# Kernel tuning notes

Hardware: AMD Instinct MI355X
Metric: run time of the kernel (lower is better)

Reference implementation:

```python
import jax, jax.numpy as jnp
import numpy as np

ALPHA = 0.5
PATH_LEN = 7  # 1 start entity + 3 (module, entity) hops
NUM_ENTITIES = 200000
EMBED = 128
NUM_MOD = 64
HIDDEN = 512
OUT_DIM = 64
BATCH = 8192


def setup_inputs() -> dict:
    key = jax.random.key(0)
    ks = jax.random.split(key, 8)
    stdv = 1.0 / np.sqrt(EMBED)
    return {
        "entity_embeds": jax.random.normal(ks[0], (NUM_ENTITIES, EMBED), jnp.float32) * 0.05,
        "W_mods": jax.random.uniform(ks[1], (NUM_MOD, EMBED, EMBED), jnp.float32, -stdv, stdv),
        "W1": jax.random.normal(ks[2], (HIDDEN, EMBED), jnp.float32) * stdv,
        "b1": jax.random.normal(ks[3], (HIDDEN,), jnp.float32) * 0.01,
        "W2": jax.random.normal(ks[4], (OUT_DIM, HIDDEN), jnp.float32) * (1.0 / np.sqrt(HIDDEN)),
        "b2": jax.random.normal(ks[5], (OUT_DIM,), jnp.float32) * 0.01,
        "entity_ids": jax.random.randint(ks[6], (BATCH, 4), 0, NUM_ENTITIES, jnp.int64 if jax.config.jax_enable_x64 else jnp.int32),
        "module_ids": jax.random.randint(ks[7], (BATCH, 3), 0, NUM_MOD, jnp.int64 if jax.config.jax_enable_x64 else jnp.int32),
    }


def reference(entity_embeds, W_mods, W1, b1, W2, b2, entity_ids, module_ids):
    # Batched version of ModuleNet.forward over a batch of fixed-length-7 paths.
    x = entity_embeds[entity_ids[:, 0]]  # [B, E] start entity embedding
    bias = x
    for h in range(3):  # hops over (module_id, entity_id) pairs
        Wm = W_mods[module_ids[:, h]]          # [B, E, E] per-row weight gather
        bias = entity_embeds[entity_ids[:, h + 1]]  # [B, E]
        x = jax.nn.relu(jnp.einsum('boi,bi->bo', Wm, x) + bias)
    w = 1.0 / (PATH_LEN * ALPHA)
    out = (1.0 - w) * bias + w * x  # [B, E]
    # classifier: Linear -> ReLU -> Linear
    h1 = jax.nn.relu(out @ W1.T + b1)
    logits = h1 @ W2.T + b2  # [B, OUT_DIM]
    return logits
```

## Files before the change

### kernel.cpp

```cpp
#include <hip/hip_runtime.h>

namespace {

typedef short bf16x8 __attribute__((ext_vector_type(8)));
typedef float f32x4 __attribute__((ext_vector_type(4)));

constexpr int BATCH = 8192;
constexpr int NMOD  = 64;
constexpr int CAP   = 256;
constexpr int CSTR  = 16;
constexpr float WB  = 1.0f / (7.0f * 0.5f);

constexpr size_t OFF_XH0 = 0;
constexpr size_t OFF_XL0 = 524288;
constexpr size_t OFF_XH1 = 1048576;
constexpr size_t OFF_XL1 = 1572864;
constexpr size_t OFF_W1H = 2097152;
constexpr size_t OFF_W1L = 2129920;
constexpr size_t OFF_W2H = 2162688;
constexpr size_t OFF_W2L = 2179072;
constexpr size_t OFF_CNT = 2195456;
constexpr size_t OFF_BKT = 2198528;

__device__ __forceinline__ ushort f2bf(float x) {
  unsigned u = __builtin_bit_cast(unsigned, x);
  u += 0x7FFFu + ((u >> 16) & 1u);
  return (ushort)(u >> 16);
}
__device__ __forceinline__ float bf2f(ushort h) {
  return __builtin_bit_cast(float, ((unsigned)h) << 16);
}
__device__ __forceinline__ void cvt8(const float* v, bf16x8& hi, bf16x8& lo) {
#pragma unroll
  for (int j = 0; j < 8; ++j) {
    const float x = v[j];
    const ushort h = f2bf(x);
    hi[j] = (short)h;
    lo[j] = (short)f2bf(x - bf2f(h));
  }
}

__global__ __launch_bounds__(256) void k_prep(const float* __restrict__ W1,
                                              const float* __restrict__ W2,
                                              const int* __restrict__ mids,
                                              float* __restrict__ ws) {
  __shared__ int wsum[4];
  const int bx = blockIdx.x;
  const int tid = threadIdx.x;
  if (bx < 48) {
    const float* src;
    ushort *dh, *dl;
    size_t i8;
    if (bx < 32) {
      src = W1; dh = (ushort*)(ws + OFF_W1H); dl = (ushort*)(ws + OFF_W1L);
      i8 = (size_t)bx * 256 + tid;
    } else {
      src = W2; dh = (ushort*)(ws + OFF_W2H); dl = (ushort*)(ws + OFF_W2L);
      i8 = (size_t)(bx - 32) * 256 + tid;
    }
    float v[8];
    *(float4*)&v[0] = *(const float4*)&src[i8 * 8];
    *(float4*)&v[4] = *(const float4*)&src[i8 * 8 + 4];
    bf16x8 hi, lo;
    cvt8(v, hi, lo);
    *(bf16x8*)&dh[i8 * 8] = hi;
    *(bf16x8*)&dl[i8 * 8] = lo;
  } else {
    const int hm = bx - 48;
    const int h = hm >> 6, m = hm & 63;
    int* cnt = (int*)(ws + OFF_CNT);
    int* bkt = (int*)(ws + OFF_BKT) + hm * CAP;
    const int wv = tid >> 6, ln = tid & 63;
    int count = 0;
    for (int it = 0; it < BATCH / 256; ++it) {
      const int b = it * 256 + tid;
      const bool hit = (mids[b * 3 + h] == m);
      const unsigned long long mask = __ballot(hit);
      const int pre = __popcll(mask & ((1ull << ln) - 1ull));
      if (ln == 0) wsum[wv] = __popcll(mask);
      __syncthreads();
      int wbase = count;
#pragma unroll
      for (int u = 0; u < 4; ++u)
        if (u < wv) wbase += wsum[u];
      if (hit) bkt[wbase + pre] = b;
      count += wsum[0] + wsum[1] + wsum[2] + wsum[3];
      __syncthreads();
    }
    if (tid == 0) cnt[hm * CSTR] = count;
  }
}

template <int HOP>
__global__ __launch_bounds__(256, 2) void k_hop(const float* __restrict__ E,
                                                const float* __restrict__ Wm,
                                                const int* __restrict__ eids,
                                                float* __restrict__ ws) {
  const int m = blockIdx.x >> 3, sl = blockIdx.x & 7;
  const int cn = ((const int*)(ws + OFF_CNT))[(HOP * NMOD + m) * CSTR];
  const int r0 = sl * 32;
  if (r0 >= cn) return;
  const int nr = min(32, cn - r0);

  __shared__ ushort wh[128 * 72];
  __shared__ ushort wl[128 * 72];
  __shared__ int rows[32], esrc[32], ebia[32];

  const int tid = threadIdx.x;
  const float* WmG = Wm + (size_t)m * 16384;
  const int* bkt = (const int*)(ws + OFF_BKT) + (HOP * NMOD + m) * CAP + r0;
  const ushort* XHp = (const ushort*)(ws + (HOP == 2 ? OFF_XH1 : OFF_XH0));
  const ushort* XLp = (const ushort*)(ws + (HOP == 2 ? OFF_XL1 : OFF_XL0));
  ushort* XHn = (ushort*)(ws + (HOP == 1 ? OFF_XH1 : OFF_XH0));
  ushort* XLn = (ushort*)(ws + (HOP == 1 ? OFF_XL1 : OFF_XL0));

  if (tid < 32) {
    const int b = bkt[tid < nr ? tid : 0];
    rows[tid] = b;
    esrc[tid] = (HOP == 0) ? eids[b * 4] : b;
    ebia[tid] = eids[b * 4 + HOP + 1];
  }

  const int w = tid >> 6, l = tid & 63;
  const int lg = l >> 4, lr = l & 15;
  const int g = w & 1, f0 = (w >> 1) * 4;
  const int row = g * 16 + lr;

  f32x4 acc[4] = {};

#pragma unroll
  for (int p = 0; p < 2; ++p) {
    __syncthreads();
    for (int e = tid; e < 128 * 8; e += 256) {
      const int c = e >> 3, s = e & 7;
      float v[8];
      const float* sp = &WmG[(size_t)c * 128 + p * 64 + s * 8];
      *(float4*)&v[0] = *(const float4*)&sp[0];
      *(float4*)&v[4] = *(const float4*)&sp[4];
      bf16x8 hi, lo;
      cvt8(v, hi, lo);
      *(bf16x8*)&wh[c * 72 + s * 8] = hi;
      *(bf16x8*)&wl[c * 72 + s * 8] = lo;
    }
    __syncthreads();

    bf16x8 ah[2], al[2];
#pragma unroll
    for (int s = 0; s < 2; ++s) {
      const int k0 = p * 64 + s * 32 + lg * 8;
      if (HOP == 0) {
        const float* sp = E + (size_t)esrc[row] * 128;
        float v[8];
        *(float4*)&v[0] = *(const float4*)&sp[k0];
        *(float4*)&v[4] = *(const float4*)&sp[k0 + 4];
        cvt8(v, ah[s], al[s]);
      } else {
        const size_t xo = (size_t)esrc[row] * 128 + k0;
        ah[s] = *(const bf16x8*)&XHp[xo];
        al[s] = *(const bf16x8*)&XLp[xo];
      }
    }

#pragma unroll
    for (int f = 0; f < 4; ++f) {
      const int c = (f0 + f) * 16 + lr;
#pragma unroll
      for (int s = 0; s < 2; ++s) {
        const bf16x8 bh = *(const bf16x8*)&wh[c * 72 + s * 32 + lg * 8];
        const bf16x8 bl = *(const bf16x8*)&wl[c * 72 + s * 32 + lg * 8];
        acc[f] = __builtin_amdgcn_mfma_f32_16x16x32_bf16(ah[s], bh, acc[f], 0, 0, 0);
        acc[f] = __builtin_amdgcn_mfma_f32_16x16x32_bf16(al[s], bh, acc[f], 0, 0, 0);
        acc[f] = __builtin_amdgcn_mfma_f32_16x16x32_bf16(ah[s], bl, acc[f], 0, 0, 0);
      }
    }
  }

#pragma unroll
  for (int q = 0; q < 4; ++q) {
    const int orow = g * 16 + lg * 4 + q;
    if (orow < nr) {
      const int b = rows[orow];
      const float* bp = E + (size_t)ebia[orow] * 128;
      const size_t ob = (size_t)b * 128;
#pragma unroll
      for (int f = 0; f < 4; ++f) {
        const int col = (f0 + f) * 16 + lr;
        const float bias = bp[col];
        float v = fmaxf(acc[f][q] + bias, 0.f);
        if (HOP == 2) v = (1.f - WB) * bias + WB * v;
        const ushort h = f2bf(v);
        XHn[ob + col] = h;
        XLn[ob + col] = f2bf(v - bf2f(h));
      }
    }
  }
}

constexpr int HSTR = 520;
__global__ __launch_bounds__(256, 2) void k_mlp(const float* __restrict__ b1,
                                                const float* __restrict__ b2,
                                                float* __restrict__ ws,
                                                float* __restrict__ out) {
  __shared__ ushort hh[16 * HSTR];
  __shared__ ushort hl[16 * HSTR];
  const int tid = threadIdx.x;
  const int row0 = blockIdx.x * 16;
  const ushort* XH = (const ushort*)(ws + OFF_XH0);
  const ushort* XL = (const ushort*)(ws + OFF_XL0);
  const ushort* W1H = (const ushort*)(ws + OFF_W1H);
  const ushort* W1L = (const ushort*)(ws + OFF_W1L);
  const ushort* W2H = (const ushort*)(ws + OFF_W2H);
  const ushort* W2L = (const ushort*)(ws + OFF_W2L);

  const int w = tid >> 6, l = tid & 63;
  const int lg = l >> 4, lr = l & 15;

  bf16x8 ah[4], al[4];
#pragma unroll
  for (int s = 0; s < 4; ++s) {
    const size_t xo = (size_t)(row0 + lr) * 128 + s * 32 + lg * 8;
    ah[s] = *(const bf16x8*)&XH[xo];
    al[s] = *(const bf16x8*)&XL[xo];
  }
  f32x4 acc[8] = {};
#pragma unroll
  for (int f = 0; f < 8; ++f) {
    const int c = w * 128 + f * 16 + lr;
#pragma unroll
    for (int s = 0; s < 4; ++s) {
      const size_t wo = (size_t)c * 128 + s * 32 + lg * 8;
      const bf16x8 bh = *(const bf16x8*)&W1H[wo];
      const bf16x8 bl = *(const bf16x8*)&W1L[wo];
      acc[f] = __builtin_amdgcn_mfma_f32_16x16x32_bf16(ah[s], bh, acc[f], 0, 0, 0);
      acc[f] = __builtin_amdgcn_mfma_f32_16x16x32_bf16(al[s], bh, acc[f], 0, 0, 0);
      acc[f] = __builtin_amdgcn_mfma_f32_16x16x32_bf16(ah[s], bl, acc[f], 0, 0, 0);
    }
  }
#pragma unroll
  for (int f = 0; f < 8; ++f) {
    const int c = w * 128 + f * 16 + lr;
    const float bb = b1[c];
#pragma unroll
    for (int q = 0; q < 4; ++q) {
      const int r = lg * 4 + q;
      const float v = fmaxf(acc[f][q] + bb, 0.f);
      const ushort h = f2bf(v);
      hh[r * HSTR + c] = h;
      hl[r * HSTR + c] = f2bf(v - bf2f(h));
    }
  }
  __syncthreads();

  f32x4 acc2 = {};
#pragma unroll 4
  for (int s = 0; s < 16; ++s) {
    const size_t wo = (size_t)(w * 16 + lr) * 512 + s * 32 + lg * 8;
    const bf16x8 a2h = *(const bf16x8*)&W2H[wo];
    const bf16x8 a2l = *(const bf16x8*)&W2L[wo];
    const int ko = s * 32 + lg * 8;
    const bf16x8 b2h = *(const bf16x8*)&hh[lr * HSTR + ko];
    const bf16x8 b2l = *(const bf16x8*)&hl[lr * HSTR + ko];
    acc2 = __builtin_amdgcn_mfma_f32_16x16x32_bf16(a2h, b2h, acc2, 0, 0, 0);
    acc2 = __builtin_amdgcn_mfma_f32_16x16x32_bf16(a2l, b2h, acc2, 0, 0, 0);
    acc2 = __builtin_amdgcn_mfma_f32_16x16x32_bf16(a2h, b2l, acc2, 0, 0, 0);
  }
  const float4 bb2 = *(const float4*)&b2[w * 16 + lg * 4];
  float4 o;
  o.x = acc2[0] + bb2.x;
  o.y = acc2[1] + bb2.y;
  o.z = acc2[2] + bb2.z;
  o.w = acc2[3] + bb2.w;
  *(float4*)&out[(size_t)(row0 + lr) * 64 + w * 16 + lg * 4] = o;
}

}

extern "C" void kernel_launch(void* const* d_in, const int* in_sizes, int n_in,
                              void* d_out, int out_size, void* d_ws,
                              size_t ws_size, hipStream_t stream) {
  const float* E  = (const float*)d_in[0];
  const float* Wm = (const float*)d_in[1];
  const float* W1 = (const float*)d_in[2];
  const float* b1 = (const float*)d_in[3];
  const float* W2 = (const float*)d_in[4];
  const float* b2 = (const float*)d_in[5];
  const int* eids = (const int*)d_in[6];
  const int* mids = (const int*)d_in[7];
  float* out = (float*)d_out;
  float* ws = (float*)d_ws;

  k_prep<<<dim3(240), dim3(256), 0, stream>>>(W1, W2, mids, ws);
  k_hop<0><<<dim3(512), dim3(256), 0, stream>>>(E, Wm, eids, ws);
  k_hop<1><<<dim3(512), dim3(256), 0, stream>>>(E, Wm, eids, ws);
  k_hop<2><<<dim3(512), dim3(256), 0, stream>>>(E, Wm, eids, ws);
  k_mlp<<<dim3(512), dim3(256), 0, stream>>>(b1, b2, ws, out);
}
```

Before: 82.25 us.

## Fuse final hop with MLP and double rows per hop block

Merges the third hop kernel with the classifier MLP, so the final path activations stay in shared memory instead of being written to and re-read from the workspace. This also removes one kernel launch. Each hop block now handles 64 rows instead of 32, which amortises the per-block fp32-to-bf16 weight conversion into shared memory over twice as many rows, using 256 blocks instead of 512. The trade-offs are fewer blocks (less parallelism and occupancy across CUs) and a serial 16-row MLP loop inside each fused block. The fused kernel also reads W1 and W2 from global memory once per 16-row group.

```diff
diff --git a/kernel.cpp b/kernel.cpp
--- a/kernel.cpp
+++ b/kernel.cpp
@@ -96,25 +96,25 @@
                                                 const float* __restrict__ Wm,
                                                 const int* __restrict__ eids,
                                                 float* __restrict__ ws) {
-  const int m = blockIdx.x >> 3, sl = blockIdx.x & 7;
+  const int m = blockIdx.x >> 2, sl = blockIdx.x & 3;
   const int cn = ((const int*)(ws + OFF_CNT))[(HOP * NMOD + m) * CSTR];
-  const int r0 = sl * 32;
+  const int r0 = sl * 64;
   if (r0 >= cn) return;
-  const int nr = min(32, cn - r0);
+  const int nr = min(64, cn - r0);
 
   __shared__ ushort wh[128 * 72];
   __shared__ ushort wl[128 * 72];
-  __shared__ int rows[32], esrc[32], ebia[32];
+  __shared__ int rows[64], esrc[64], ebia[64];
 
   const int tid = threadIdx.x;
   const float* WmG = Wm + (size_t)m * 16384;
   const int* bkt = (const int*)(ws + OFF_BKT) + (HOP * NMOD + m) * CAP + r0;
-  const ushort* XHp = (const ushort*)(ws + (HOP == 2 ? OFF_XH1 : OFF_XH0));
-  const ushort* XLp = (const ushort*)(ws + (HOP == 2 ? OFF_XL1 : OFF_XL0));
-  ushort* XHn = (ushort*)(ws + (HOP == 1 ? OFF_XH1 : OFF_XH0));
-  ushort* XLn = (ushort*)(ws + (HOP == 1 ? OFF_XL1 : OFF_XL0));
-
-  if (tid < 32) {
+  const ushort* XHp = (const ushort*)(ws + OFF_XH0);
+  const ushort* XLp = (const ushort*)(ws + OFF_XL0);
+  ushort* XHn = (ushort*)(ws + (HOP == 0 ? OFF_XH0 : OFF_XH1));
+  ushort* XLn = (ushort*)(ws + (HOP == 0 ? OFF_XL0 : OFF_XL1));
+
+  if (tid < 64) {
     const int b = bkt[tid < nr ? tid : 0];
     rows[tid] = b;
     esrc[tid] = (HOP == 0) ? eids[b * 4] : b;
@@ -123,10 +123,9 @@
 
   const int w = tid >> 6, l = tid & 63;
   const int lg = l >> 4, lr = l & 15;
-  const int g = w & 1, f0 = (w >> 1) * 4;
-  const int row = g * 16 + lr;
-
-  f32x4 acc[4] = {};
+  const int g0 = (w & 1) * 2, f0 = (w >> 1) * 4;
+
+  f32x4 acc[2][4] = {};
 
 #pragma unroll
   for (int p = 0; p < 2; ++p) {
@@ -144,20 +143,24 @@
     }
     __syncthreads();
 
-    bf16x8 ah[2], al[2];
-#pragma unroll
-    for (int s = 0; s < 2; ++s) {
-      const int k0 = p * 64 + s * 32 + lg * 8;
-      if (HOP == 0) {
-        const float* sp = E + (size_t)esrc[row] * 128;
-        float v[8];
-        *(float4*)&v[0] = *(const float4*)&sp[k0];
-        *(float4*)&v[4] = *(const float4*)&sp[k0 + 4];
-        cvt8(v, ah[s], al[s]);
-      } else {
-        const size_t xo = (size_t)esrc[row] * 128 + k0;
-        ah[s] = *(const bf16x8*)&XHp[xo];
-        al[s] = *(const bf16x8*)&XLp[xo];
+    bf16x8 ah[2][2], al[2][2];
+#pragma unroll
+    for (int g = 0; g < 2; ++g) {
+      const int row = (g0 + g) * 16 + lr;
+#pragma unroll
+      for (int s = 0; s < 2; ++s) {
+        const int k0 = p * 64 + s * 32 + lg * 8;
+        if (HOP == 0) {
+          const float* sp = E + (size_t)esrc[row] * 128;
+          float v[8];
+          *(float4*)&v[0] = *(const float4*)&sp[k0];
+          *(float4*)&v[4] = *(const float4*)&sp[k0 + 4];
+          cvt8(v, ah[g][s], al[g][s]);
+        } else {
+          const size_t xo = (size_t)esrc[row] * 128 + k0;
+          ah[g][s] = *(const bf16x8*)&XHp[xo];
+          al[g][s] = *(const bf16x8*)&XLp[xo];
+        }
       }
     }
 
@@ -168,109 +171,212 @@
       for (int s = 0; s < 2; ++s) {
         const bf16x8 bh = *(const bf16x8*)&wh[c * 72 + s * 32 + lg * 8];
         const bf16x8 bl = *(const bf16x8*)&wl[c * 72 + s * 32 + lg * 8];
-        acc[f] = __builtin_amdgcn_mfma_f32_16x16x32_bf16(ah[s], bh, acc[f], 0, 0, 0);
-        acc[f] = __builtin_amdgcn_mfma_f32_16x16x32_bf16(al[s], bh, acc[f], 0, 0, 0);
-        acc[f] = __builtin_amdgcn_mfma_f32_16x16x32_bf16(ah[s], bl, acc[f], 0, 0, 0);
-      }
-    }
-  }
-
-#pragma unroll
-  for (int q = 0; q < 4; ++q) {
-    const int orow = g * 16 + lg * 4 + q;
-    if (orow < nr) {
-      const int b = rows[orow];
-      const float* bp = E + (size_t)ebia[orow] * 128;
-      const size_t ob = (size_t)b * 128;
-#pragma unroll
-      for (int f = 0; f < 4; ++f) {
-        const int col = (f0 + f) * 16 + lr;
-        const float bias = bp[col];
-        float v = fmaxf(acc[f][q] + bias, 0.f);
-        if (HOP == 2) v = (1.f - WB) * bias + WB * v;
-        const ushort h = f2bf(v);
-        XHn[ob + col] = h;
-        XLn[ob + col] = f2bf(v - bf2f(h));
-      }
-    }
-  }
-}
-
-constexpr int HSTR = 520;
-__global__ __launch_bounds__(256, 2) void k_mlp(const float* __restrict__ b1,
-                                                const float* __restrict__ b2,
-                                                float* __restrict__ ws,
-                                                float* __restrict__ out) {
-  __shared__ ushort hh[16 * HSTR];
-  __shared__ ushort hl[16 * HSTR];
+#pragma unroll
+        for (int g = 0; g < 2; ++g) {
+          acc[g][f] = __builtin_amdgcn_mfma_f32_16x16x32_bf16(ah[g][s], bh, acc[g][f], 0, 0, 0);
+          acc[g][f] = __builtin_amdgcn_mfma_f32_16x16x32_bf16(al[g][s], bh, acc[g][f], 0, 0, 0);
+          acc[g][f] = __builtin_amdgcn_mfma_f32_16x16x32_bf16(ah[g][s], bl, acc[g][f], 0, 0, 0);
+        }
+      }
+    }
+  }
+
+#pragma unroll
+  for (int g = 0; g < 2; ++g) {
+#pragma unroll
+    for (int q = 0; q < 4; ++q) {
+      const int row = (g0 + g) * 16 + lg * 4 + q;
+      if (row < nr) {
+        const int b = rows[row];
+        const float* bp = E + (size_t)ebia[row] * 128;
+        const size_t ob = (size_t)b * 128;
+#pragma unroll
+        for (int f = 0; f < 4; ++f) {
+          const int col = (f0 + f) * 16 + lr;
+          const float bias = bp[col];
+          const float v = fmaxf(acc[g][f][q] + bias, 0.f);
+          const ushort h = f2bf(v);
+          XHn[ob + col] = h;
+          XLn[ob + col] = f2bf(v - bf2f(h));
+        }
+      }
+    }
+  }
+}
+
+__global__ __launch_bounds__(256, 2) void k_hopmlp(
+    const float* __restrict__ E, const float* __restrict__ Wm,
+    const float* __restrict__ b1, const float* __restrict__ b2,
+    const int* __restrict__ eids, float* __restrict__ ws,
+    float* __restrict__ out) {
+  const int m = blockIdx.x >> 2, sl = blockIdx.x & 3;
+  const int cn = ((const int*)(ws + OFF_CNT))[(2 * NMOD + m) * CSTR];
+  const int r0 = sl * 64;
+  if (r0 >= cn) return;
+  const int nr = min(64, cn - r0);
+
+  __shared__ __align__(16) char smem[72448];
+  ushort* wh = (ushort*)smem;
+  ushort* wl = wh + 128 * 72;
+  ushort* hh = (ushort*)smem;
+  ushort* hl = hh + 16 * 520;
+  ushort* xh = (ushort*)(smem + 36864);
+  ushort* xl = xh + 64 * 136;
+  int* rows = (int*)(smem + 71680);
+  int* ebia = rows + 64;
+
   const int tid = threadIdx.x;
-  const int row0 = blockIdx.x * 16;
-  const ushort* XH = (const ushort*)(ws + OFF_XH0);
-  const ushort* XL = (const ushort*)(ws + OFF_XL0);
+  const float* WmG = Wm + (size_t)m * 16384;
+  const int* bkt = (const int*)(ws + OFF_BKT) + (2 * NMOD + m) * CAP + r0;
+  const ushort* XHp = (const ushort*)(ws + OFF_XH1);
+  const ushort* XLp = (const ushort*)(ws + OFF_XL1);
   const ushort* W1H = (const ushort*)(ws + OFF_W1H);
   const ushort* W1L = (const ushort*)(ws + OFF_W1L);
   const ushort* W2H = (const ushort*)(ws + OFF_W2H);
   const ushort* W2L = (const ushort*)(ws + OFF_W2L);
 
+  if (tid < 64) {
+    const int b = bkt[tid < nr ? tid : 0];
+    rows[tid] = b;
+    ebia[tid] = eids[b * 4 + 3];
+  }
+
   const int w = tid >> 6, l = tid & 63;
   const int lg = l >> 4, lr = l & 15;
-
-  bf16x8 ah[4], al[4];
-#pragma unroll
-  for (int s = 0; s < 4; ++s) {
-    const size_t xo = (size_t)(row0 + lr) * 128 + s * 32 + lg * 8;
-    ah[s] = *(const bf16x8*)&XH[xo];
-    al[s] = *(const bf16x8*)&XL[xo];
-  }
-  f32x4 acc[8] = {};
-#pragma unroll
-  for (int f = 0; f < 8; ++f) {
-    const int c = w * 128 + f * 16 + lr;
+  const int g0 = (w & 1) * 2, f0 = (w >> 1) * 4;
+
+  f32x4 acc[2][4] = {};
+#pragma unroll
+  for (int p = 0; p < 2; ++p) {
+    __syncthreads();
+    for (int e = tid; e < 128 * 8; e += 256) {
+      const int c = e >> 3, s = e & 7;
+      float v[8];
+      const float* sp = &WmG[(size_t)c * 128 + p * 64 + s * 8];
+      *(float4*)&v[0] = *(const float4*)&sp[0];
+      *(float4*)&v[4] = *(const float4*)&sp[4];
+      bf16x8 hi, lo;
+      cvt8(v, hi, lo);
+      *(bf16x8*)&wh[c * 72 + s * 8] = hi;
+      *(bf16x8*)&wl[c * 72 + s * 8] = lo;
+    }
+    __syncthreads();
+
+    bf16x8 ah[2][2], al[2][2];
+#pragma unroll
+    for (int g = 0; g < 2; ++g) {
+      const int row = (g0 + g) * 16 + lr;
+#pragma unroll
+      for (int s = 0; s < 2; ++s) {
+        const size_t xo = (size_t)rows[row] * 128 + p * 64 + s * 32 + lg * 8;
+        ah[g][s] = *(const bf16x8*)&XHp[xo];
+        al[g][s] = *(const bf16x8*)&XLp[xo];
+      }
+    }
+
+#pragma unroll
+    for (int f = 0; f < 4; ++f) {
+      const int c = (f0 + f) * 16 + lr;
+#pragma unroll
+      for (int s = 0; s < 2; ++s) {
+        const bf16x8 bh = *(const bf16x8*)&wh[c * 72 + s * 32 + lg * 8];
+        const bf16x8 bl = *(const bf16x8*)&wl[c * 72 + s * 32 + lg * 8];
+#pragma unroll
+        for (int g = 0; g < 2; ++g) {
+          acc[g][f] = __builtin_amdgcn_mfma_f32_16x16x32_bf16(ah[g][s], bh, acc[g][f], 0, 0, 0);
+          acc[g][f] = __builtin_amdgcn_mfma_f32_16x16x32_bf16(al[g][s], bh, acc[g][f], 0, 0, 0);
+          acc[g][f] = __builtin_amdgcn_mfma_f32_16x16x32_bf16(ah[g][s], bl, acc[g][f], 0, 0, 0);
+        }
+      }
+    }
+  }
+
+#pragma unroll
+  for (int g = 0; g < 2; ++g) {
+#pragma unroll
+    for (int q = 0; q < 4; ++q) {
+      const int row = (g0 + g) * 16 + lg * 4 + q;
+      if (row < nr) {
+        const float* bp = E + (size_t)ebia[row] * 128;
+#pragma unroll
+        for (int f = 0; f < 4; ++f) {
+          const int col = (f0 + f) * 16 + lr;
+          const float bias = bp[col];
+          float v = fmaxf(acc[g][f][q] + bias, 0.f);
+          v = (1.f - WB) * bias + WB * v;
+          const ushort h = f2bf(v);
+          xh[row * 136 + col] = h;
+          xl[row * 136 + col] = f2bf(v - bf2f(h));
+        }
+      }
+    }
+  }
+  __syncthreads();
+
+  for (int p4 = 0; p4 < 4; ++p4) {
+    if (p4 * 16 >= nr) break;
+    bf16x8 ah[4], al[4];
 #pragma unroll
     for (int s = 0; s < 4; ++s) {
-      const size_t wo = (size_t)c * 128 + s * 32 + lg * 8;
-      const bf16x8 bh = *(const bf16x8*)&W1H[wo];
-      const bf16x8 bl = *(const bf16x8*)&W1L[wo];
-      acc[f] = __builtin_amdgcn_mfma_f32_16x16x32_bf16(ah[s], bh, acc[f], 0, 0, 0);
-      acc[f] = __builtin_amdgcn_mfma_f32_16x16x32_bf16(al[s], bh, acc[f], 0, 0, 0);
-      acc[f] = __builtin_amdgcn_mfma_f32_16x16x32_bf16(ah[s], bl, acc[f], 0, 0, 0);
-    }
-  }
-#pragma unroll
-  for (int f = 0; f < 8; ++f) {
-    const int c = w * 128 + f * 16 + lr;
-    const float bb = b1[c];
-#pragma unroll
-    for (int q = 0; q < 4; ++q) {
-      const int r = lg * 4 + q;
-      const float v = fmaxf(acc[f][q] + bb, 0.f);
-      const ushort h = f2bf(v);
-      hh[r * HSTR + c] = h;
-      hl[r * HSTR + c] = f2bf(v - bf2f(h));
-    }
-  }
-  __syncthreads();
-
-  f32x4 acc2 = {};
+      const int xo = (p4 * 16 + lr) * 136 + s * 32 + lg * 8;
+      ah[s] = *(const bf16x8*)&xh[xo];
+      al[s] = *(const bf16x8*)&xl[xo];
+    }
+    f32x4 acc1[8] = {};
+#pragma unroll
+    for (int f = 0; f < 8; ++f) {
+      const int c = w * 128 + f * 16 + lr;
+#pragma unroll
+      for (int s = 0; s < 4; ++s) {
+        const size_t wo = (size_t)c * 128 + s * 32 + lg * 8;
+        const bf16x8 bh = *(const bf16x8*)&W1H[wo];
+        const bf16x8 bl = *(const bf16x8*)&W1L[wo];
+        acc1[f] = __builtin_amdgcn_mfma_f32_16x16x32_bf16(ah[s], bh, acc1[f], 0, 0, 0);
+        acc1[f] = __builtin_amdgcn_mfma_f32_16x16x32_bf16(al[s], bh, acc1[f], 0, 0, 0);
+        acc1[f] = __builtin_amdgcn_mfma_f32_16x16x32_bf16(ah[s], bl, acc1[f], 0, 0, 0);
+      }
+    }
+#pragma unroll
+    for (int f = 0; f < 8; ++f) {
+      const int c = w * 128 + f * 16 + lr;
+      const float bb = b1[c];
+#pragma unroll
+      for (int q = 0; q < 4; ++q) {
+        const int r = lg * 4 + q;
+        const float v = fmaxf(acc1[f][q] + bb, 0.f);
+        const ushort h = f2bf(v);
+        hh[r * 520 + c] = h;
+        hl[r * 520 + c] = f2bf(v - bf2f(h));
+      }
+    }
+    __syncthreads();
+
+    f32x4 acc2 = {};
 #pragma unroll 4
-  for (int s = 0; s < 16; ++s) {
-    const size_t wo = (size_t)(w * 16 + lr) * 512 + s * 32 + lg * 8;
-    const bf16x8 a2h = *(const bf16x8*)&W2H[wo];
-    const bf16x8 a2l = *(const bf16x8*)&W2L[wo];
-    const int ko = s * 32 + lg * 8;
-    const bf16x8 b2h = *(const bf16x8*)&hh[lr * HSTR + ko];
-    const bf16x8 b2l = *(const bf16x8*)&hl[lr * HSTR + ko];
-    acc2 = __builtin_amdgcn_mfma_f32_16x16x32_bf16(a2h, b2h, acc2, 0, 0, 0);
-    acc2 = __builtin_amdgcn_mfma_f32_16x16x32_bf16(a2l, b2h, acc2, 0, 0, 0);
-    acc2 = __builtin_amdgcn_mfma_f32_16x16x32_bf16(a2h, b2l, acc2, 0, 0, 0);
-  }
-  const float4 bb2 = *(const float4*)&b2[w * 16 + lg * 4];
-  float4 o;
-  o.x = acc2[0] + bb2.x;
-  o.y = acc2[1] + bb2.y;
-  o.z = acc2[2] + bb2.z;
-  o.w = acc2[3] + bb2.w;
-  *(float4*)&out[(size_t)(row0 + lr) * 64 + w * 16 + lg * 4] = o;
+    for (int s = 0; s < 16; ++s) {
+      const size_t wo = (size_t)(w * 16 + lr) * 512 + s * 32 + lg * 8;
+      const bf16x8 a2h = *(const bf16x8*)&W2H[wo];
+      const bf16x8 a2l = *(const bf16x8*)&W2L[wo];
+      const int ko = s * 32 + lg * 8;
+      const bf16x8 b2h = *(const bf16x8*)&hh[lr * 520 + ko];
+      const bf16x8 b2l = *(const bf16x8*)&hl[lr * 520 + ko];
+      acc2 = __builtin_amdgcn_mfma_f32_16x16x32_bf16(a2h, b2h, acc2, 0, 0, 0);
+      acc2 = __builtin_amdgcn_mfma_f32_16x16x32_bf16(a2l, b2h, acc2, 0, 0, 0);
+      acc2 = __builtin_amdgcn_mfma_f32_16x16x32_bf16(a2h, b2l, acc2, 0, 0, 0);
+    }
+    const int lrow = p4 * 16 + lr;
+    if (lrow < nr) {
+      const int b = rows[lrow];
+      const float4 bb2 = *(const float4*)&b2[w * 16 + lg * 4];
+      float4 o;
+      o.x = acc2[0] + bb2.x;
+      o.y = acc2[1] + bb2.y;
+      o.z = acc2[2] + bb2.z;
+      o.w = acc2[3] + bb2.w;
+      *(float4*)&out[(size_t)b * 64 + w * 16 + lg * 4] = o;
+    }
+    __syncthreads();
+  }
 }
 
 }
@@ -290,8 +396,7 @@
   float* ws = (float*)d_ws;
 
   k_prep<<<dim3(240), dim3(256), 0, stream>>>(W1, W2, mids, ws);
-  k_hop<0><<<dim3(512), dim3(256), 0, stream>>>(E, Wm, eids, ws);
-  k_hop<1><<<dim3(512), dim3(256), 0, stream>>>(E, Wm, eids, ws);
-  k_hop<2><<<dim3(512), dim3(256), 0, stream>>>(E, Wm, eids, ws);
-  k_mlp<<<dim3(512), dim3(256), 0, stream>>>(b1, b2, ws, out);
-}
+  k_hop<0><<<dim3(256), dim3(256), 0, stream>>>(E, Wm, eids, ws);
+  k_hop<1><<<dim3(256), dim3(256), 0, stream>>>(E, Wm, eids, ws);
+  k_hopmlp<<<dim3(256), dim3(256), 0, stream>>>(E, Wm, b1, b2, eids, ws, out);
+}
```

Result: slower. 111.0 us (+35.0%).
